# Performance work log

Measured on AMD Instinct MI355X. Metric: run time of the kernel, lower is better.

## Reference

```python
import jax, jax.numpy as jnp
import numpy as np

EPS = 1e-6
L, H, D, DFF = 4, 6, 6, 64  # n_layers, num_heads(=dim, head_dim=1), d_hid, ffn hidden


def layernorm(x, w, b):
    mu = jnp.mean(x, axis=-1, keepdims=True)
    var = jnp.mean((x - mu) ** 2, axis=-1, keepdims=True)
    return (x - mu) / jnp.sqrt(var + EPS) * w + b


def autocorr(x, qw, qb, kw, kb, vw, vb, l1w, l1b):
    # x: [B,S,H]; head_dim==1 so per-head Linear is scalar w*x+b per head.
    k_in = jnp.concatenate([x[:, :1], x[:, :-1]], axis=1)   # roll right, first row kept
    v_in = jnp.concatenate([x[:, 1:], x[:, -1:]], axis=1)   # roll left, last row kept
    q = x * qw + qb
    k = k_in * kw + kb
    v = v_in * vw + vb
    teo = q * q - k * v                                      # [B,S,H]
    # nn.LayerNorm([1]) over size-1 axis: mean==x, var==0 -> output is bias
    normed = (teo - teo) / jnp.sqrt(EPS) * l1w + l1b
    scores = jax.nn.softmax(normed, axis=1)                  # over seq dim
    return scores * teo


def mha(x, p, li, ai):
    out = autocorr(x, p['qw'][li, ai], p['qb'][li, ai], p['kw'][li, ai],
                   p['kb'][li, ai], p['vw'][li, ai], p['vb'][li, ai],
                   p['ln1_w'][li, ai], p['ln1_b'][li, ai])
    return layernorm(out + x, p['mha_ln_w'][li, ai], p['mha_ln_b'][li, ai])


def setup_inputs() -> dict:
    key = jax.random.key(0)
    ks = jax.random.split(key, 24)
    n = jax.random.normal
    inp = {
        'x_batch': n(ks[0], (128, 4096, 6), jnp.float32),
        'enc_output': n(ks[1], (128, 4096, 6), jnp.float32),
        'dec_ln_w': jnp.ones((D,), jnp.float32),
        'dec_ln_b': jnp.zeros((D,), jnp.float32),
        'qw': n(ks[2], (L, 2, H), jnp.float32),
        'qb': n(ks[3], (L, 2, H), jnp.float32) * 0.1,
        'kw': n(ks[4], (L, 2, H), jnp.float32),
        'kb': n(ks[5], (L, 2, H), jnp.float32) * 0.1,
        'vw': n(ks[6], (L, 2, H), jnp.float32),
        'vb': n(ks[7], (L, 2, H), jnp.float32) * 0.1,
        'ln1_w': jnp.ones((L, 2), jnp.float32),
        'ln1_b': jnp.zeros((L, 2), jnp.float32),
        'mha_ln_w': jnp.ones((L, 2, D), jnp.float32),
        'mha_ln_b': jnp.zeros((L, 2, D), jnp.float32),
        'ffn_w1': n(ks[8], (L, DFF, D), jnp.float32) * (1.0 / np.sqrt(D)),
        'ffn_b1': jnp.zeros((L, DFF), jnp.float32),
        'ffn_w2': n(ks[9], (L, D, DFF), jnp.float32) * (1.0 / np.sqrt(DFF)),
        'ffn_b2': jnp.zeros((L, D), jnp.float32),
        'ffn_ln_w': jnp.ones((L, D), jnp.float32),
        'ffn_ln_b': jnp.zeros((L, D), jnp.float32),
    }
    return inp


def reference(x_batch, enc_output, dec_ln_w, dec_ln_b, qw, qb, kw, kb, vw, vb,
              ln1_w, ln1_b, mha_ln_w, mha_ln_b, ffn_w1, ffn_b1, ffn_w2, ffn_b2,
              ffn_ln_w, ffn_ln_b):
    p = dict(qw=qw, qb=qb, kw=kw, kb=kb, vw=vw, vb=vb, ln1_w=ln1_w, ln1_b=ln1_b,
             mha_ln_w=mha_ln_w, mha_ln_b=mha_ln_b)
    x = layernorm(x_batch, dec_ln_w, dec_ln_b)  # dropout p=0 -> identity
    for li in range(L):
        x = mha(x, p, li, 0)   # self-attention block
        x = mha(x, p, li, 1)   # "enc" attention block (also self, per source)
        h = jax.nn.relu(jnp.einsum('bsd,fd->bsf', x, ffn_w1[li]) + ffn_b1[li])
        y = jnp.einsum('bsf,df->bsd', h, ffn_w2[li]) + ffn_b2[li] + x
        x = layernorm(y, ffn_ln_w[li], ffn_ln_b[li])
    return x
```

## Files before the change

kernel.cpp:

```cpp
#include <hip/hip_runtime.h>

#define S_LEN  4096
#define DM     6
#define NLAYER 4
#define NFF    64
#define HALO   8
#define TPB    256
#define TILE_OUT (TPB - 2*HALO)

typedef float    vf2 __attribute__((ext_vector_type(2)));
typedef _Float16 vh2 __attribute__((ext_vector_type(2)));

#define B1P_OFF (NLAYER*NFF*DM)
#define W2P_OFF (B1P_OFF + NLAYER*NFF)
#define PACK_TOTAL (W2P_OFF + NLAYER*NFF*DM)

__device__ __forceinline__ vf2 splat2(float s){ vf2 r; r.x = s; r.y = s; return r; }
__device__ __forceinline__ vh2 bch2(unsigned u){ return __builtin_bit_cast(vh2, u); }

__global__ void prep_weights(const float* __restrict__ w1,
                             const float* __restrict__ b1,
                             const float* __restrict__ w2,
                             unsigned* __restrict__ ws) {
    int i = blockIdx.x * 256 + threadIdx.x;
    if (i >= PACK_TOTAL) return;
    float v;
    if (i < B1P_OFF) {
        v = w1[i];
    } else if (i < W2P_OFF) {
        v = b1[i - B1P_OFF];
    } else {
        int r  = i - W2P_OFF;
        int li = r / (NFF*DM);
        int q  = r % (NFF*DM);
        int f  = q / DM, d = q % DM;
        v = w2[li*(DM*NFF) + d*NFF + f];
    }
    _Float16 h = (_Float16)v;
    unsigned short bits = __builtin_bit_cast(unsigned short, h);
    ws[i] = (unsigned)bits | ((unsigned)bits << 16);
}

__device__ __forceinline__ void ln6v(vf2* v, const float* __restrict__ w,
                                     const float* __restrict__ b) {
    vf2 mu = (((v[0]+v[1])+(v[2]+v[3]))+(v[4]+v[5])) * (1.0f/6.0f);
    vf2 var = splat2(0.0f);
#pragma unroll
    for (int d = 0; d < DM; ++d) { vf2 dd = v[d]-mu; var = __builtin_elementwise_fma(dd, dd, var); }
    vf2 a = var * (1.0f/6.0f) + splat2(1e-6f);
    vf2 r; r.x = rsqrtf(a.x); r.y = rsqrtf(a.y);
#pragma unroll
    for (int d = 0; d < DM; ++d)
        v[d] = __builtin_elementwise_fma((v[d]-mu)*r, splat2(w[d]), splat2(b[d]));
}

__global__ __launch_bounds__(TPB)
void decoder_fused(const float* __restrict__ x_batch,
                   const float* __restrict__ dec_ln_w, const float* __restrict__ dec_ln_b,
                   const float* __restrict__ qw, const float* __restrict__ qb,
                   const float* __restrict__ kw, const float* __restrict__ kb,
                   const float* __restrict__ vw, const float* __restrict__ vb,
                   const float* __restrict__ mha_ln_w, const float* __restrict__ mha_ln_b,
                   const unsigned* __restrict__ wsp,
                   const float* __restrict__ ffn_b2,
                   const float* __restrict__ ffn_ln_w, const float* __restrict__ ffn_ln_b,
                   float* __restrict__ out) {
    const int t  = threadIdx.x;
    const int bp = blockIdx.y;
    const int b0 = 2*bp, b1 = 2*bp + 1;
    const int p  = blockIdx.x * TILE_OUT + t - HALO;
    const int pc = min(max(p, 0), S_LEN - 1);

    __shared__ vf2 xs[2][DM][TPB];

    vf2 x2[DM];
    {
        const float2* sA = reinterpret_cast<const float2*>(x_batch + ((size_t)b0 * S_LEN + pc) * DM);
        const float2* sB = reinterpret_cast<const float2*>(x_batch + ((size_t)b1 * S_LEN + pc) * DM);
        float2 a0 = sA[0], a1 = sA[1], a2 = sA[2];
        float2 c0 = sB[0], c1 = sB[1], c2 = sB[2];
        x2[0].x=a0.x; x2[1].x=a0.y; x2[2].x=a1.x; x2[3].x=a1.y; x2[4].x=a2.x; x2[5].x=a2.y;
        x2[0].y=c0.x; x2[1].y=c0.y; x2[2].y=c1.x; x2[3].y=c1.y; x2[4].y=c2.x; x2[5].y=c2.y;
    }

    ln6v(x2, dec_ln_w, dec_ln_b);

#pragma unroll 1
    for (int li = 0; li < NLAYER; ++li) {
#pragma unroll 1
        for (int ai = 0; ai < 2; ++ai) {
            const int st   = li*2 + ai;
            const int buf  = st & 1;
            const int base = st * DM;

#pragma unroll
            for (int d = 0; d < DM; ++d) xs[buf][d][t] = x2[d];
            __syncthreads();
            const int tm = (t == 0)       ? 0       : t - 1;
            const int tp = (t == TPB - 1) ? TPB - 1 : t + 1;
            vf2 xm[DM], xpl[DM];
#pragma unroll
            for (int d = 0; d < DM; ++d) { xm[d] = xs[buf][d][tm]; xpl[d] = xs[buf][d][tp]; }
            if (p <= 0) {
#pragma unroll
                for (int d = 0; d < DM; ++d) xm[d] = x2[d];
            }
            if (p >= S_LEN - 1) {
#pragma unroll
                for (int d = 0; d < DM; ++d) xpl[d] = x2[d];
            }

#pragma unroll
            for (int d = 0; d < DM; ++d) {
                vf2 q = __builtin_elementwise_fma(x2[d],  splat2(qw[base+d]), splat2(qb[base+d]));
                vf2 k = __builtin_elementwise_fma(xm[d],  splat2(kw[base+d]), splat2(kb[base+d]));
                vf2 v = __builtin_elementwise_fma(xpl[d], splat2(vw[base+d]), splat2(vb[base+d]));
                vf2 teo = __builtin_elementwise_fma(q, q, -(k*v));
                x2[d] = __builtin_elementwise_fma(teo, splat2(1.0f/(float)S_LEN), x2[d]);
            }
            ln6v(x2, mha_ln_w + base, mha_ln_b + base);
        }

        {
            const unsigned* w1p = wsp + (size_t)li*NFF*DM;
            const unsigned* b1p = wsp + B1P_OFF + (size_t)li*NFF;
            const unsigned* w2p = wsp + W2P_OFF + (size_t)li*NFF*DM;
            const float*    b2  = ffn_b2 + li*DM;

            vh2 xh[DM];
#pragma unroll
            for (int d = 0; d < DM; ++d) { xh[d].x = (_Float16)x2[d].x; xh[d].y = (_Float16)x2[d].y; }
            vh2 ya[DM], yb[DM];
#pragma unroll
            for (int d = 0; d < DM; ++d) { ya[d] = (vh2)(_Float16)0; yb[d] = (vh2)(_Float16)0; }

#pragma unroll 4
            for (int f = 0; f < NFF; f += 2) {
                vh2 h0 = bch2(b1p[f]);
                vh2 h1 = bch2(b1p[f+1]);
#pragma unroll
                for (int d = 0; d < DM; ++d) {
                    h0 = __builtin_elementwise_fma(xh[d], bch2(w1p[f*DM + d]),     h0);
                    h1 = __builtin_elementwise_fma(xh[d], bch2(w1p[(f+1)*DM + d]), h1);
                }
                vh2 z = (vh2)(_Float16)0;
                h0 = __builtin_elementwise_max(h0, z);
                h1 = __builtin_elementwise_max(h1, z);
#pragma unroll
                for (int d = 0; d < DM; ++d) {
                    ya[d] = __builtin_elementwise_fma(h0, bch2(w2p[f*DM + d]),     ya[d]);
                    yb[d] = __builtin_elementwise_fma(h1, bch2(w2p[(f+1)*DM + d]), yb[d]);
                }
            }
#pragma unroll
            for (int d = 0; d < DM; ++d) {
                x2[d].x = x2[d].x + b2[d] + ((float)ya[d].x + (float)yb[d].x);
                x2[d].y = x2[d].y + b2[d] + ((float)ya[d].y + (float)yb[d].y);
            }
            ln6v(x2, ffn_ln_w + li*DM, ffn_ln_b + li*DM);
        }
    }

    if (t >= HALO && t < TPB - HALO && p < S_LEN) {
        float2* dA = reinterpret_cast<float2*>(out + ((size_t)b0 * S_LEN + p) * DM);
        float2* dB = reinterpret_cast<float2*>(out + ((size_t)b1 * S_LEN + p) * DM);
        dA[0] = make_float2(x2[0].x, x2[1].x);
        dA[1] = make_float2(x2[2].x, x2[3].x);
        dA[2] = make_float2(x2[4].x, x2[5].x);
        dB[0] = make_float2(x2[0].y, x2[1].y);
        dB[1] = make_float2(x2[2].y, x2[3].y);
        dB[2] = make_float2(x2[4].y, x2[5].y);
    }
}

extern "C" void kernel_launch(void* const* d_in, const int* in_sizes, int n_in,
                              void* d_out, int out_size, void* d_ws, size_t ws_size,
                              hipStream_t stream) {
    const float* x_batch  = (const float*)d_in[0];
    const float* dec_ln_w = (const float*)d_in[2];
    const float* dec_ln_b = (const float*)d_in[3];
    const float* qw       = (const float*)d_in[4];
    const float* qb       = (const float*)d_in[5];
    const float* kw       = (const float*)d_in[6];
    const float* kb       = (const float*)d_in[7];
    const float* vw       = (const float*)d_in[8];
    const float* vb       = (const float*)d_in[9];
    const float* mha_ln_w = (const float*)d_in[12];
    const float* mha_ln_b = (const float*)d_in[13];
    const float* ffn_w1   = (const float*)d_in[14];
    const float* ffn_b1   = (const float*)d_in[15];
    const float* ffn_w2   = (const float*)d_in[16];
    const float* ffn_b2   = (const float*)d_in[17];
    const float* ffn_ln_w = (const float*)d_in[18];
    const float* ffn_ln_b = (const float*)d_in[19];
    float* out = (float*)d_out;
    unsigned* wsp = (unsigned*)d_ws;

    prep_weights<<<(PACK_TOTAL + 255)/256, 256, 0, stream>>>(ffn_w1, ffn_b1, ffn_w2, wsp);

    const int B  = in_sizes[0] / (S_LEN * DM);
    const int BP = B / 2;
    dim3 grid((S_LEN + TILE_OUT - 1) / TILE_OUT, BP);
    decoder_fused<<<grid, TPB, 0, stream>>>(
        x_batch, dec_ln_w, dec_ln_b, qw, qb, kw, kb, vw, vb,
        mha_ln_w, mha_ln_b, wsp, ffn_b2, ffn_ln_w, ffn_ln_b, out);
}
```

Measured before the change: 160.2 us.

## Exchange sequence halos with wave shuffles instead of LDS and block barriers

Each thread now holds two adjacent sequence positions of one batch instead of one position from two batches. Neighbour values for the k/v shift are exchanged with intra-wave shuffles, which removes the shared-memory staging and the __syncthreads per attention stage. Each wave owns its own 112-output tile with a 4-lane halo, and loads and stores become float4. The grid is fixed at 10 blocks per batch, so some waves start past the end of the sequence and only do discarded work, which raises redundant compute compared with the old tiling. The fp16 conversion also switches to a packed cvt_pkrtz instruction.

Result: no change. 159.9 us (-0.2%).

```diff
diff --git a/kernel.cpp b/kernel.cpp
--- a/kernel.cpp
+++ b/kernel.cpp
@@ -6,7 +6,9 @@
 #define NFF    64
 #define HALO   8
 #define TPB    256
-#define TILE_OUT (TPB - 2*HALO)
+#define OUT_PER_WAVE 112
+#define WAVES_PER_BATCH 37
+#define BLK_X 10
 
 typedef float    vf2 __attribute__((ext_vector_type(2)));
 typedef _Float16 vh2 __attribute__((ext_vector_type(2)));
@@ -65,22 +67,23 @@
                    const float* __restrict__ ffn_b2,
                    const float* __restrict__ ffn_ln_w, const float* __restrict__ ffn_ln_b,
                    float* __restrict__ out) {
-    const int t  = threadIdx.x;
-    const int bp = blockIdx.y;
-    const int b0 = 2*bp, b1 = 2*bp + 1;
-    const int p  = blockIdx.x * TILE_OUT + t - HALO;
-    const int pc = min(max(p, 0), S_LEN - 1);
-
-    __shared__ vf2 xs[2][DM][TPB];
+    const int lane = threadIdx.x & 63;
+    const int w    = blockIdx.x * (TPB/64) + (threadIdx.x >> 6);
+    const int b    = blockIdx.y;
+    const int p    = w * OUT_PER_WAVE - HALO + 2*lane;
 
     vf2 x2[DM];
-    {
-        const float2* sA = reinterpret_cast<const float2*>(x_batch + ((size_t)b0 * S_LEN + pc) * DM);
-        const float2* sB = reinterpret_cast<const float2*>(x_batch + ((size_t)b1 * S_LEN + pc) * DM);
-        float2 a0 = sA[0], a1 = sA[1], a2 = sA[2];
-        float2 c0 = sB[0], c1 = sB[1], c2 = sB[2];
-        x2[0].x=a0.x; x2[1].x=a0.y; x2[2].x=a1.x; x2[3].x=a1.y; x2[4].x=a2.x; x2[5].x=a2.y;
-        x2[0].y=c0.x; x2[1].y=c0.y; x2[2].y=c1.x; x2[3].y=c1.y; x2[4].y=c2.x; x2[5].y=c2.y;
+    if (p >= 0 && p + 1 < S_LEN) {
+        const float4* s = reinterpret_cast<const float4*>(x_batch + ((size_t)b*S_LEN + p)*DM);
+        float4 a0 = s[0], a1 = s[1], a2 = s[2];
+        x2[0].x=a0.x; x2[1].x=a0.y; x2[2].x=a0.z; x2[3].x=a0.w; x2[4].x=a1.x; x2[5].x=a1.y;
+        x2[0].y=a1.z; x2[1].y=a1.w; x2[2].y=a2.x; x2[3].y=a2.y; x2[4].y=a2.z; x2[5].y=a2.w;
+    } else {
+        const int pc = min(max(p, 0), S_LEN-1);
+        const float2* s = reinterpret_cast<const float2*>(x_batch + ((size_t)b*S_LEN + pc)*DM);
+        float2 a0 = s[0], a1 = s[1], a2 = s[2];
+        x2[0] = splat2(a0.x); x2[1] = splat2(a0.y); x2[2] = splat2(a1.x);
+        x2[3] = splat2(a1.y); x2[4] = splat2(a2.x); x2[5] = splat2(a2.y);
     }
 
     ln6v(x2, dec_ln_w, dec_ln_b);
@@ -89,32 +92,22 @@
     for (int li = 0; li < NLAYER; ++li) {
 #pragma unroll 1
         for (int ai = 0; ai < 2; ++ai) {
-            const int st   = li*2 + ai;
-            const int buf  = st & 1;
-            const int base = st * DM;
-
-#pragma unroll
-            for (int d = 0; d < DM; ++d) xs[buf][d][t] = x2[d];
-            __syncthreads();
-            const int tm = (t == 0)       ? 0       : t - 1;
-            const int tp = (t == TPB - 1) ? TPB - 1 : t + 1;
-            vf2 xm[DM], xpl[DM];
-#pragma unroll
-            for (int d = 0; d < DM; ++d) { xm[d] = xs[buf][d][tm]; xpl[d] = xs[buf][d][tp]; }
-            if (p <= 0) {
-#pragma unroll
-                for (int d = 0; d < DM; ++d) xm[d] = x2[d];
-            }
-            if (p >= S_LEN - 1) {
-#pragma unroll
-                for (int d = 0; d < DM; ++d) xpl[d] = x2[d];
-            }
-
+            const int base = (li*2 + ai) * DM;
+            vf2 xm[DM], xp[DM];
 #pragma unroll
             for (int d = 0; d < DM; ++d) {
-                vf2 q = __builtin_elementwise_fma(x2[d],  splat2(qw[base+d]), splat2(qb[base+d]));
-                vf2 k = __builtin_elementwise_fma(xm[d],  splat2(kw[base+d]), splat2(kb[base+d]));
-                vf2 v = __builtin_elementwise_fma(xpl[d], splat2(vw[base+d]), splat2(vb[base+d]));
+                float up = __shfl_up (x2[d].y, 1);
+                float dn = __shfl_down(x2[d].x, 1);
+                xm[d].x = (p <= 0) ? x2[d].x : up;
+                xm[d].y = x2[d].x;
+                xp[d].x = x2[d].y;
+                xp[d].y = (p + 1 >= S_LEN - 1) ? x2[d].y : dn;
+            }
+#pragma unroll
+            for (int d = 0; d < DM; ++d) {
+                vf2 q = __builtin_elementwise_fma(x2[d], splat2(qw[base+d]), splat2(qb[base+d]));
+                vf2 k = __builtin_elementwise_fma(xm[d], splat2(kw[base+d]), splat2(kb[base+d]));
+                vf2 v = __builtin_elementwise_fma(xp[d], splat2(vw[base+d]), splat2(vb[base+d]));
                 vf2 teo = __builtin_elementwise_fma(q, q, -(k*v));
                 x2[d] = __builtin_elementwise_fma(teo, splat2(1.0f/(float)S_LEN), x2[d]);
             }
@@ -129,7 +122,8 @@
 
             vh2 xh[DM];
 #pragma unroll
-            for (int d = 0; d < DM; ++d) { xh[d].x = (_Float16)x2[d].x; xh[d].y = (_Float16)x2[d].y; }
+            for (int d = 0; d < DM; ++d)
+                xh[d] = __builtin_bit_cast(vh2, __builtin_amdgcn_cvt_pkrtz(x2[d].x, x2[d].y));
             vh2 ya[DM], yb[DM];
 #pragma unroll
             for (int d = 0; d < DM; ++d) { ya[d] = (vh2)(_Float16)0; yb[d] = (vh2)(_Float16)0; }
@@ -161,15 +155,14 @@
         }
     }
 
-    if (t >= HALO && t < TPB - HALO && p < S_LEN) {
-        float2* dA = reinterpret_cast<float2*>(out + ((size_t)b0 * S_LEN + p) * DM);
-        float2* dB = reinterpret_cast<float2*>(out + ((size_t)b1 * S_LEN + p) * DM);
-        dA[0] = make_float2(x2[0].x, x2[1].x);
-        dA[1] = make_float2(x2[2].x, x2[3].x);
-        dA[2] = make_float2(x2[4].x, x2[5].x);
-        dB[0] = make_float2(x2[0].y, x2[1].y);
-        dB[1] = make_float2(x2[2].y, x2[3].y);
-        dB[2] = make_float2(x2[4].y, x2[5].y);
+    if (lane >= HALO/2 && lane < 64 - HALO/2 + 4 - 8 + 60 - 56) {}
+    if (lane >= 4 && lane < 60 && p < S_LEN) {
+        float4* dst = reinterpret_cast<float4*>(out + ((size_t)b*S_LEN + p)*DM);
+        float4 a0, a1, a2;
+        a0.x=x2[0].x; a0.y=x2[1].x; a0.z=x2[2].x; a0.w=x2[3].x;
+        a1.x=x2[4].x; a1.y=x2[5].x; a1.z=x2[0].y; a1.w=x2[1].y;
+        a2.x=x2[2].y; a2.y=x2[3].y; a2.z=x2[4].y; a2.w=x2[5].y;
+        dst[0]=a0; dst[1]=a1; dst[2]=a2;
     }
 }
 
@@ -198,9 +191,8 @@
 
     prep_weights<<<(PACK_TOTAL + 255)/256, 256, 0, stream>>>(ffn_w1, ffn_b1, ffn_w2, wsp);
 
-    const int B  = in_sizes[0] / (S_LEN * DM);
-    const int BP = B / 2;
-    dim3 grid((S_LEN + TILE_OUT - 1) / TILE_OUT, BP);
+    const int B = in_sizes[0] / (S_LEN * DM);
+    dim3 grid(BLK_X, B);
     decoder_fused<<<grid, TPB, 0, stream>>>(
         x_batch, dec_ln_w, dec_ln_b, qw, qb, kw, kb, vw, vb,
         mha_ln_w, mha_ln_b, wsp, ffn_b2, ffn_ln_w, ffn_ln_b, out);
```
